# Performance work log

Measured on AMD Instinct MI355X. Metric: run time of the kernel, lower is better.

Reference implementation:

```python
import jax, jax.numpy as jnp
import numpy as np

B = 65536
G = 9          # grid_size
C = 10         # num_classes
BS = 3         # block_size = sqrt(grid_size)
CONSTRAINT_WEIGHT = 0.1


def setup_inputs() -> dict:
    key = jax.random.key(0)
    k1, k2, k3 = jax.random.split(key, 3)
    logits = jax.random.normal(k1, (B, G, G, C), dtype=jnp.float32)
    targets = jax.random.randint(k2, (B, G, G), 0, C)
    puzzles = jax.random.randint(k3, (B, G, G), 0, C)
    return {"logits": logits, "targets": targets, "puzzles": puzzles}


def _sudoku_loss(logits, targets, puzzles):
    mask = (puzzles == 0).astype(logits.dtype)               # [B, G, G]

    # --- masked cross-entropy over empty cells ---
    logp = jax.nn.log_softmax(logits, axis=-1)               # [B, G, G, C]
    ce = -jnp.take_along_axis(logp, targets[..., None], axis=-1)[..., 0]
    ce_loss = (ce * mask).sum() / (mask.sum() + 1e-8)

    # --- constraint loss (rows, cols, 3x3 boxes), fully vectorized ---
    probs = jnp.exp(logp)                                    # softmax probs
    wp = probs * mask[..., None]                             # [B, G, G, C]

    def group_mse(digit_sums, msum):
        # digit_sums: [B, G_groups, C]; msum: [B, G_groups]
        # torch: per-group F.mse_loss over [B, C-1], summed over groups
        target = msum[..., None] / G                         # [B, Gg, 1]
        diff = digit_sums[..., 1:] - target                  # [B, Gg, C-1]
        return (diff * diff).mean(axis=(0, 2)).sum()

    # rows: sum over columns (axis 2)
    row_loss = group_mse(wp.sum(axis=2), mask.sum(axis=2))
    # cols: sum over rows (axis 1)
    col_loss = group_mse(wp.sum(axis=1), mask.sum(axis=1))
    # boxes: reshape to [B, bi, ri, bj, cj, C], sum within-box dims
    box_ds = wp.reshape(B, BS, BS, BS, BS, C).sum(axis=(2, 4)).reshape(B, G, C)
    box_ms = mask.reshape(B, BS, BS, BS, BS).sum(axis=(2, 4)).reshape(B, G)
    box_loss = group_mse(box_ds, box_ms)

    num_constraints = G * 2 + BS * BS                        # 27
    constraint_loss = (row_loss + col_loss + box_loss) / num_constraints

    # torch wraps the constraint loss in torch.tensor(...), detaching it
    total = ce_loss + CONSTRAINT_WEIGHT * jax.lax.stop_gradient(constraint_loss)
    return total, ce_loss, constraint_loss


def reference(logits, targets, puzzles):
    total, ce_loss, constraint_loss = _sudoku_loss(logits, targets, puzzles)
    return total, ce_loss, constraint_loss
```

## Files before the change

kernel.cpp:

```cpp
#include <hip/hip_runtime.h>


constexpr int kB    = 65536;
constexpr int PPB   = 6;
constexpr int TPB   = 512;
constexpr int NSLOT = 256;
constexpr int SLOT_STRIDE = 16;
constexpr int CSTRIDE = 12;

__global__ __launch_bounds__(TPB) void sudoku_main(
    const float* __restrict__ logits,
    const int*   __restrict__ targets,
    const int*   __restrict__ puzzles,
    float*       __restrict__ ws)
{
    __shared__ __align__(16) float probs[TPB * CSTRIDE];
    __shared__ float red[3][TPB / 64];

    const int tid    = threadIdx.x;
    const int pzbase = blockIdx.x * PPB;
    const int q      = tid / 81;

    float ce = 0.f, mcnt = 0.f;
    float wv[10];
    #pragma unroll
    for (int c = 0; c < 10; ++c) wv[c] = 0.f;

    const bool active = (q < PPB) && (pzbase + q < kB);
    if (active) {
        const int idx = pzbase * 81 + tid;
        const int pz = puzzles[idx];

        if (pz == 0) {
            const int tg = targets[idx];
            const float* xp = logits + (size_t)idx * 10;
            float2 v0 = *(const float2*)(xp + 0);
            float2 v1 = *(const float2*)(xp + 2);
            float2 v2 = *(const float2*)(xp + 4);
            float2 v3 = *(const float2*)(xp + 6);
            float2 v4 = *(const float2*)(xp + 8);
            float x[10];
            x[0]=v0.x; x[1]=v0.y; x[2]=v1.x; x[3]=v1.y; x[4]=v2.x;
            x[5]=v2.y; x[6]=v3.x; x[7]=v3.y; x[8]=v4.x; x[9]=v4.y;

            float mx = x[0];
            #pragma unroll
            for (int c = 1; c < 10; ++c) mx = fmaxf(mx, x[c]);
            float e[10];
            float S = 0.f;
            #pragma unroll
            for (int c = 0; c < 10; ++c) { e[c] = __expf(x[c] - mx); S += e[c]; }
            const float inv = 1.0f / S;

            float xt = x[0];
            #pragma unroll
            for (int c = 1; c < 10; ++c) xt = (tg == c) ? x[c] : xt;
            ce   = mx + __logf(S) - xt;
            mcnt = 1.f;
            wv[0] = 1.f;
            #pragma unroll
            for (int c = 1; c < 10; ++c) wv[c] = e[c] * inv;
        }
    }
    {
        float* dst = &probs[tid * CSTRIDE];
        *(float4*)(dst + 0) = make_float4(wv[0], wv[1], wv[2], wv[3]);
        *(float4*)(dst + 4) = make_float4(wv[4], wv[5], wv[6], wv[7]);
        *(float2*)(dst + 8) = make_float2(wv[8], wv[9]);
    }
    __syncthreads();

    float diff2 = 0.f;
    if (tid < PPB * 27) {
        float s[10];
        #pragma unroll
        for (int c = 0; c < 10; ++c) s[c] = 0.f;

        if (tid < PPB * 9) {
            const int q2 = tid / 9, r = tid - q2 * 9;
            const float* base = &probs[(q2 * 81 + r * 9) * CSTRIDE];
            #pragma unroll
            for (int i = 0; i < 9; ++i) {
                const float* cell = base + i * CSTRIDE;
                const float4 a = *(const float4*)(cell + 0);
                const float4 b = *(const float4*)(cell + 4);
                const float2 c2 = *(const float2*)(cell + 8);
                s[0]+=a.x; s[1]+=a.y; s[2]+=a.z; s[3]+=a.w;
                s[4]+=b.x; s[5]+=b.y; s[6]+=b.z; s[7]+=b.w;
                s[8]+=c2.x; s[9]+=c2.y;
            }
        } else if (tid < PPB * 18) {
            const int u = tid - PPB * 9;
            const int q2 = u / 9, j = u - q2 * 9;
            const float* base = &probs[(q2 * 81 + j) * CSTRIDE];
            #pragma unroll
            for (int i = 0; i < 9; ++i) {
                const float* cell = base + i * (9 * CSTRIDE);
                const float4 a = *(const float4*)(cell + 0);
                const float4 b = *(const float4*)(cell + 4);
                const float2 c2 = *(const float2*)(cell + 8);
                s[0]+=a.x; s[1]+=a.y; s[2]+=a.z; s[3]+=a.w;
                s[4]+=b.x; s[5]+=b.y; s[6]+=b.z; s[7]+=b.w;
                s[8]+=c2.x; s[9]+=c2.y;
            }
        } else {
            const int u = tid - PPB * 18;
            const int q2 = u / 9, b = u - q2 * 9;
            const int br = b / 3, bc = b - br * 3;
            const float* base = &probs[(q2 * 81 + br * 27 + bc * 3) * CSTRIDE];
            #pragma unroll
            for (int dr = 0; dr < 3; ++dr) {
                #pragma unroll
                for (int dc = 0; dc < 3; ++dc) {
                    const float* cell = base + (dr * 9 + dc) * CSTRIDE;
                    const float4 a = *(const float4*)(cell + 0);
                    const float4 bb = *(const float4*)(cell + 4);
                    const float2 c2 = *(const float2*)(cell + 8);
                    s[0]+=a.x; s[1]+=a.y; s[2]+=a.z; s[3]+=a.w;
                    s[4]+=bb.x; s[5]+=bb.y; s[6]+=bb.z; s[7]+=bb.w;
                    s[8]+=c2.x; s[9]+=c2.y;
                }
            }
        }
        const float tm = s[0] * (1.f / 9.f);
        #pragma unroll
        for (int c = 1; c < 10; ++c) { const float d = s[c] - tm; diff2 += d * d; }
    }

    #pragma unroll
    for (int off = 32; off > 0; off >>= 1) {
        diff2 += __shfl_down(diff2, off);
        ce    += __shfl_down(ce, off);
        mcnt  += __shfl_down(mcnt, off);
    }
    const int wave = tid >> 6;
    if ((tid & 63) == 0) { red[0][wave] = diff2; red[1][wave] = ce; red[2][wave] = mcnt; }
    __syncthreads();
    if (tid == 0) {
        float d = 0.f, c2 = 0.f, m = 0.f;
        #pragma unroll
        for (int w = 0; w < TPB / 64; ++w) { d += red[0][w]; c2 += red[1][w]; m += red[2][w]; }
        float* slot = ws + (size_t)(blockIdx.x & (NSLOT - 1)) * SLOT_STRIDE;
        atomicAdd(&slot[0], d);
        atomicAdd(&slot[1], c2);
        atomicAdd(&slot[2], m);
    }
}

__global__ void sudoku_final(const float* __restrict__ ws, float* __restrict__ out)
{
    const int t = threadIdx.x;
    float d = 0.f, c2 = 0.f, m = 0.f;
    for (int s = t; s < NSLOT; s += 64) {
        const float* sl = ws + (size_t)s * SLOT_STRIDE;
        d += sl[0]; c2 += sl[1]; m += sl[2];
    }
    #pragma unroll
    for (int off = 32; off > 0; off >>= 1) {
        d  += __shfl_down(d, off);
        c2 += __shfl_down(c2, off);
        m  += __shfl_down(m, off);
    }
    if (t == 0) {
        const float ce_loss = c2 / (m + 1e-8f);
        const float constraint = d / ((float)kB * 9.f * 27.f);
        out[0] = ce_loss + 0.1f * constraint;
        out[1] = ce_loss;
        out[2] = constraint;
    }
}

extern "C" void kernel_launch(void* const* d_in, const int* in_sizes, int n_in,
                              void* d_out, int out_size, void* d_ws, size_t ws_size,
                              hipStream_t stream)
{
    const float* logits  = (const float*)d_in[0];
    const int*   targets = (const int*)d_in[1];
    const int*   puzzles = (const int*)d_in[2];
    float* ws  = (float*)d_ws;
    float* out = (float*)d_out;

    hipMemsetAsync(d_ws, 0, NSLOT * SLOT_STRIDE * sizeof(float), stream);

    const int blocks = (kB + PPB - 1) / PPB;
    sudoku_main<<<blocks, TPB, 0, stream>>>(logits, targets, puzzles, ws);
    sudoku_final<<<1, 64, 0, stream>>>(ws, out);
}
```

Measured before the change: 354.0 us.

## Switch to persistent blocks looping over puzzle rounds with prefetched puzzle masks

```diff
diff --git a/kernel.cpp b/kernel.cpp
--- a/kernel.cpp
+++ b/kernel.cpp
@@ -1,14 +1,17 @@
 #include <hip/hip_runtime.h>
 
 
-constexpr int kB    = 65536;
-constexpr int PPB   = 6;
-constexpr int TPB   = 512;
-constexpr int NSLOT = 256;
+constexpr int kB     = 65536;
+constexpr int TPB    = 512;
+constexpr int NBLK   = 1024;
+constexpr int PPBLK  = kB / NBLK;
+constexpr int PPB_R  = 6;
+constexpr int ROUNDS = (PPBLK + PPB_R - 1) / PPB_R;
+constexpr int NSLOT  = 256;
 constexpr int SLOT_STRIDE = 16;
 constexpr int CSTRIDE = 12;
 
-__global__ __launch_bounds__(TPB) void sudoku_main(
+__global__ __launch_bounds__(TPB, 8) void sudoku_main(
     const float* __restrict__ logits,
     const int*   __restrict__ targets,
     const int*   __restrict__ puzzles,
@@ -17,23 +20,32 @@
     __shared__ __align__(16) float probs[TPB * CSTRIDE];
     __shared__ float red[3][TPB / 64];
 
-    const int tid    = threadIdx.x;
-    const int pzbase = blockIdx.x * PPB;
-    const int q      = tid / 81;
-
-    float ce = 0.f, mcnt = 0.f;
-    float wv[10];
-    #pragma unroll
-    for (int c = 0; c < 10; ++c) wv[c] = 0.f;
-
-    const bool active = (q < PPB) && (pzbase + q < kB);
-    if (active) {
-        const int idx = pzbase * 81 + tid;
-        const int pz = puzzles[idx];
-
-        if (pz == 0) {
+    const int  tid  = threadIdx.x;
+    const int  q    = tid / 81;
+    const bool actq = (q < PPB_R);
+    const size_t blkbase = (size_t)blockIdx.x * PPBLK * 81;
+
+    float ce = 0.f, mcnt = 0.f, diff2 = 0.f;
+
+    int pz_cur = 1;
+    if (actq) pz_cur = puzzles[blkbase + tid];
+
+    for (int r = 0; r < ROUNDS; ++r) {
+        int pz_next = 1;
+        if (r + 1 < ROUNDS) {
+            const bool actn = actq && ((r + 1) * PPB_R + q < PPBLK);
+            if (actn) pz_next = puzzles[blkbase + (size_t)(r + 1) * (PPB_R * 81) + tid];
+        }
+
+        const bool act = actq && (r * PPB_R + q < PPBLK);
+        float wv[10];
+        #pragma unroll
+        for (int c = 0; c < 10; ++c) wv[c] = 0.f;
+
+        if (act && pz_cur == 0) {
+            const size_t idx = blkbase + (size_t)r * (PPB_R * 81) + tid;
             const int tg = targets[idx];
-            const float* xp = logits + (size_t)idx * 10;
+            const float* xp = logits + idx * 10;
             float2 v0 = *(const float2*)(xp + 0);
             float2 v1 = *(const float2*)(xp + 2);
             float2 v2 = *(const float2*)(xp + 4);
@@ -55,76 +67,79 @@
             float xt = x[0];
             #pragma unroll
             for (int c = 1; c < 10; ++c) xt = (tg == c) ? x[c] : xt;
-            ce   = mx + __logf(S) - xt;
-            mcnt = 1.f;
+            ce   += mx + __logf(S) - xt;
+            mcnt += 1.f;
             wv[0] = 1.f;
             #pragma unroll
             for (int c = 1; c < 10; ++c) wv[c] = e[c] * inv;
         }
-    }
-    {
-        float* dst = &probs[tid * CSTRIDE];
-        *(float4*)(dst + 0) = make_float4(wv[0], wv[1], wv[2], wv[3]);
-        *(float4*)(dst + 4) = make_float4(wv[4], wv[5], wv[6], wv[7]);
-        *(float2*)(dst + 8) = make_float2(wv[8], wv[9]);
-    }
-    __syncthreads();
-
-    float diff2 = 0.f;
-    if (tid < PPB * 27) {
-        float s[10];
-        #pragma unroll
-        for (int c = 0; c < 10; ++c) s[c] = 0.f;
-
-        if (tid < PPB * 9) {
-            const int q2 = tid / 9, r = tid - q2 * 9;
-            const float* base = &probs[(q2 * 81 + r * 9) * CSTRIDE];
-            #pragma unroll
-            for (int i = 0; i < 9; ++i) {
-                const float* cell = base + i * CSTRIDE;
-                const float4 a = *(const float4*)(cell + 0);
-                const float4 b = *(const float4*)(cell + 4);
-                const float2 c2 = *(const float2*)(cell + 8);
-                s[0]+=a.x; s[1]+=a.y; s[2]+=a.z; s[3]+=a.w;
-                s[4]+=b.x; s[5]+=b.y; s[6]+=b.z; s[7]+=b.w;
-                s[8]+=c2.x; s[9]+=c2.y;
-            }
-        } else if (tid < PPB * 18) {
-            const int u = tid - PPB * 9;
-            const int q2 = u / 9, j = u - q2 * 9;
-            const float* base = &probs[(q2 * 81 + j) * CSTRIDE];
-            #pragma unroll
-            for (int i = 0; i < 9; ++i) {
-                const float* cell = base + i * (9 * CSTRIDE);
-                const float4 a = *(const float4*)(cell + 0);
-                const float4 b = *(const float4*)(cell + 4);
-                const float2 c2 = *(const float2*)(cell + 8);
-                s[0]+=a.x; s[1]+=a.y; s[2]+=a.z; s[3]+=a.w;
-                s[4]+=b.x; s[5]+=b.y; s[6]+=b.z; s[7]+=b.w;
-                s[8]+=c2.x; s[9]+=c2.y;
-            }
-        } else {
-            const int u = tid - PPB * 18;
-            const int q2 = u / 9, b = u - q2 * 9;
-            const int br = b / 3, bc = b - br * 3;
-            const float* base = &probs[(q2 * 81 + br * 27 + bc * 3) * CSTRIDE];
-            #pragma unroll
-            for (int dr = 0; dr < 3; ++dr) {
+
+        {
+            float* dst = &probs[tid * CSTRIDE];
+            *(float4*)(dst + 0) = make_float4(wv[0], wv[1], wv[2], wv[3]);
+            *(float4*)(dst + 4) = make_float4(wv[4], wv[5], wv[6], wv[7]);
+            *(float2*)(dst + 8) = make_float2(wv[8], wv[9]);
+        }
+        __syncthreads();
+
+        if (tid < PPB_R * 27) {
+            float s[10];
+            #pragma unroll
+            for (int c = 0; c < 10; ++c) s[c] = 0.f;
+
+            if (tid < PPB_R * 9) {
+                const int q2 = tid / 9, rr = tid - q2 * 9;
+                const float* base = &probs[(q2 * 81 + rr * 9) * CSTRIDE];
                 #pragma unroll
-                for (int dc = 0; dc < 3; ++dc) {
-                    const float* cell = base + (dr * 9 + dc) * CSTRIDE;
+                for (int i = 0; i < 9; ++i) {
+                    const float* cell = base + i * CSTRIDE;
                     const float4 a = *(const float4*)(cell + 0);
-                    const float4 bb = *(const float4*)(cell + 4);
+                    const float4 b = *(const float4*)(cell + 4);
                     const float2 c2 = *(const float2*)(cell + 8);
                     s[0]+=a.x; s[1]+=a.y; s[2]+=a.z; s[3]+=a.w;
-                    s[4]+=bb.x; s[5]+=bb.y; s[6]+=bb.z; s[7]+=bb.w;
+                    s[4]+=b.x; s[5]+=b.y; s[6]+=b.z; s[7]+=b.w;
                     s[8]+=c2.x; s[9]+=c2.y;
                 }
+            } else if (tid < PPB_R * 18) {
+                const int u = tid - PPB_R * 9;
+                const int q2 = u / 9, j = u - q2 * 9;
+                const float* base = &probs[(q2 * 81 + j) * CSTRIDE];
+                #pragma unroll
+                for (int i = 0; i < 9; ++i) {
+                    const float* cell = base + i * (9 * CSTRIDE);
+                    const float4 a = *(const float4*)(cell + 0);
+                    const float4 b = *(const float4*)(cell + 4);
+                    const float2 c2 = *(const float2*)(cell + 8);
+                    s[0]+=a.x; s[1]+=a.y; s[2]+=a.z; s[3]+=a.w;
+                    s[4]+=b.x; s[5]+=b.y; s[6]+=b.z; s[7]+=b.w;
+                    s[8]+=c2.x; s[9]+=c2.y;
+                }
+            } else {
+                const int u = tid - PPB_R * 18;
+                const int q2 = u / 9, b = u - q2 * 9;
+                const int br = b / 3, bc = b - br * 3;
+                const float* base = &probs[(q2 * 81 + br * 27 + bc * 3) * CSTRIDE];
+                #pragma unroll
+                for (int dr = 0; dr < 3; ++dr) {
+                    #pragma unroll
+                    for (int dc = 0; dc < 3; ++dc) {
+                        const float* cell = base + (dr * 9 + dc) * CSTRIDE;
+                        const float4 a = *(const float4*)(cell + 0);
+                        const float4 bb = *(const float4*)(cell + 4);
+                        const float2 c2 = *(const float2*)(cell + 8);
+                        s[0]+=a.x; s[1]+=a.y; s[2]+=a.z; s[3]+=a.w;
+                        s[4]+=bb.x; s[5]+=bb.y; s[6]+=bb.z; s[7]+=bb.w;
+                        s[8]+=c2.x; s[9]+=c2.y;
+                    }
+                }
             }
-        }
-        const float tm = s[0] * (1.f / 9.f);
-        #pragma unroll
-        for (int c = 1; c < 10; ++c) { const float d = s[c] - tm; diff2 += d * d; }
+            const float tm = s[0] * (1.f / 9.f);
+            #pragma unroll
+            for (int c = 1; c < 10; ++c) { const float d = s[c] - tm; diff2 += d * d; }
+        }
+        __syncthreads();
+
+        pz_cur = pz_next;
     }
 
     #pragma unroll
@@ -182,7 +197,6 @@
 
     hipMemsetAsync(d_ws, 0, NSLOT * SLOT_STRIDE * sizeof(float), stream);
 
-    const int blocks = (kB + PPB - 1) / PPB;
-    sudoku_main<<<blocks, TPB, 0, stream>>>(logits, targets, puzzles, ws);
+    sudoku_main<<<NBLK, TPB, 0, stream>>>(logits, targets, puzzles, ws);
     sudoku_final<<<1, 64, 0, stream>>>(ws, out);
 }
```

Result: faster. 295.7 us (-16.5%).
